# Kernel optimization log

Measured on AMD Instinct MI355X. Metric: run time of the kernel, lower is better.

Reference implementation:

```python
import jax, jax.numpy as jnp
import numpy as np

B, U, D, SKIP = 2048, 1024, 1024, 24

def setup_inputs() -> dict:
    key = jax.random.key(0)
    ks = jax.random.split(key, 8)
    return {
        "inputs": jax.random.normal(ks[0], (B, D), dtype=jnp.float32),
        "h_tm1": jax.random.normal(ks[1], (B, 4 * U), dtype=jnp.float32),
        "c_tm1": jax.random.normal(ks[2], (B, U), dtype=jnp.float32),
        "step": jnp.zeros((B, 1), dtype=jnp.float32),
        "prev_h": jax.random.normal(ks[3], (B, U * SKIP), dtype=jnp.float32),
        "kernel": jax.random.normal(ks[4], (D, 4 * U), dtype=jnp.float32) * (1.0 / np.sqrt(D)),
        "recurrent_kernel": jax.random.normal(ks[5], (U, 4 * U), dtype=jnp.float32) * (1.0 / np.sqrt(U)),
        "kernel2": jax.random.normal(ks[6], (U, U), dtype=jnp.float32) * (1.0 / np.sqrt(U)),
        "bias": jnp.zeros((4 * U,), dtype=jnp.float32),
        "bias2": jnp.zeros((U,), dtype=jnp.float32),
        "s0": jnp.float32(0.5),
    }

def reference(inputs, h_tm1, c_tm1, step, prev_h, kernel, recurrent_kernel, kernel2, bias, bias2, s0):
    units = kernel2.shape[0]
    # split previous 'h' state into its four gate-history blocks [B, U] each
    h_parts = jnp.stack(jnp.split(h_tm1, 4, axis=1), axis=0)          # [4, B, U]
    rk = recurrent_kernel.reshape(units, 4, units)                     # [U, 4, U]
    # fused per-gate recurrent matmuls: r[g] = h_parts[g] @ recurrent_kernel[:, g*U:(g+1)*U]
    r = jnp.einsum('gbu,ugv->gbv', h_parts, rk)                        # [4, B, U]
    x = inputs @ kernel + bias                                         # [B, 4U]
    x_i, x_f, x_c, x_o = jnp.split(x, 4, axis=1)
    i = jax.nn.sigmoid(x_i + r[0])
    f = jax.nn.sigmoid(x_f + r[1])
    c = f * c_tm1 + i * jnp.tanh(x_c + r[2])
    o = jax.nn.sigmoid(x_o + r[3])
    h = o * jnp.tanh(c)
    new_h_skip = jax.nn.sigmoid(prev_h[:, :units] @ kernel2 + bias2)
    h = s0 * h + new_h_skip * (1 - s0)
    new_h_tm1 = jnp.concatenate([i, f, c, o], axis=1)
    new_prev_h = jnp.concatenate([prev_h[:, units:], h], axis=1)
    return (h, new_h_tm1, c, step + 1, new_prev_h)
```

## Files before the change

kernel.cpp:

```cpp
#include <hip/hip_runtime.h>
#include <hip/hip_bf16.h>
#include <stdint.h>

#define BB 2048
#define UU 1024
#define SKIPN 24

typedef __attribute__((ext_vector_type(8))) short short8;
typedef __attribute__((ext_vector_type(4))) float f32x4;
typedef __attribute__((ext_vector_type(4))) unsigned short ushort4_t;

static __device__ __forceinline__ float sigmoidf_(float x) {
    return 1.0f / (1.0f + __expf(-x));
}

static __device__ __forceinline__ void load_lds16(const void* g, void* l) {
    __builtin_amdgcn_global_load_lds((const __attribute__((address_space(1))) void*)g,
                                     (__attribute__((address_space(3))) void*)l, 16, 0, 0);
}

static __device__ __forceinline__ f32x4 ntl(const f32x4* p) {
    return __builtin_nontemporal_load(p);
}
static __device__ __forceinline__ void nts(f32x4* p, f32x4 v) {
    __builtin_nontemporal_store(v, p);
}

__global__ __launch_bounds__(256) void prep(
    const float* __restrict__ inputs, const float* __restrict__ h_tm1,
    const float* __restrict__ prev_h, const float* __restrict__ kernel,
    const float* __restrict__ rkernel, const float* __restrict__ kernel2,
    __hip_bfloat16* __restrict__ kt, __hip_bfloat16* __restrict__ rkt,
    __hip_bfloat16* __restrict__ k2t, __hip_bfloat16* __restrict__ xin,
    __hip_bfloat16* __restrict__ hb, __hip_bfloat16* __restrict__ ph0) {
    const int bid = blockIdx.x;
    if (bid < 9216) {
        __shared__ float tile[32][33];
        const float* src;
        __hip_bfloat16* dst;
        int C, local;
        if (bid < 4096)      { src = kernel;  dst = kt;  C = 4096; local = bid; }
        else if (bid < 8192) { src = rkernel; dst = rkt; C = 4096; local = bid - 4096; }
        else                 { src = kernel2; dst = k2t; C = 1024; local = bid - 8192; }
        const int xt = (C == 4096) ? 128 : 32;
        const int bc = (local % xt) * 32;
        const int br = (local / xt) * 32;
        const int tx = threadIdx.x & 31, ty = threadIdx.x >> 5;
#pragma unroll
        for (int i = 0; i < 32; i += 8)
            tile[ty + i][tx] = src[(size_t)(br + ty + i) * C + bc + tx];
        __syncthreads();
#pragma unroll
        for (int i = 0; i < 32; i += 8)
            dst[(size_t)(bc + ty + i) * 1024 + br + tx] = __float2bfloat16(tile[tx][ty + i]);
    } else {
        const int idx = (bid - 9216) * 256 + threadIdx.x;
        const float* src;
        __hip_bfloat16* dst;
        int off;
        if (idx < 524288) { dst = xin; off = idx; src = inputs + (size_t)off * 4; }
        else if (idx < 2621440) { off = idx - 524288; dst = hb; src = h_tm1 + (size_t)off * 4; }
        else {
            const int i = idx - 2621440;
            const int b = i >> 8, c4 = i & 255;
            off = i; dst = ph0;
            src = prev_h + (size_t)b * (UU * SKIPN) + c4 * 4;
        }
        const float4 v = *(const float4*)src;
        union { __hip_bfloat16 h[4]; ushort4_t u; } cv;
        cv.h[0] = __float2bfloat16(v.x);
        cv.h[1] = __float2bfloat16(v.y);
        cv.h[2] = __float2bfloat16(v.z);
        cv.h[3] = __float2bfloat16(v.w);
        *(ushort4_t*)(dst + (size_t)off * 4) = cv.u;
    }
}

__global__ __launch_bounds__(256) void mega5(
    const __hip_bfloat16* __restrict__ xin,
    const __hip_bfloat16* __restrict__ hb,
    const __hip_bfloat16* __restrict__ ph0,
    const __hip_bfloat16* __restrict__ kt,
    const __hip_bfloat16* __restrict__ rkt,
    const __hip_bfloat16* __restrict__ k2t,
    const float* __restrict__ prev_h, float* __restrict__ out_prev,
    __hip_bfloat16* __restrict__ pre) {
    const int bid = blockIdx.x;
    if (bid >= 640) {
        const int b = bid - 640;
        const f32x4* s = (const f32x4*)(prev_h + (size_t)b * 24576 + 1024);
        f32x4* d = (f32x4*)(out_prev + (size_t)b * 24576);
        int c = threadIdx.x;
#pragma unroll 1
        for (int it = 0; it < 5; ++it) {
            f32x4 v0 = ntl(s + c);
            f32x4 v1 = ntl(s + c + 256);
            f32x4 v2 = ntl(s + c + 512);
            f32x4 v3 = ntl(s + c + 768);
            nts(d + c, v0);
            nts(d + c + 256, v1);
            nts(d + c + 512, v2);
            nts(d + c + 768, v3);
            c += 1024;
        }
        {
            f32x4 v0 = ntl(s + c);
            f32x4 v1 = ntl(s + c + 256);
            f32x4 v2 = ntl(s + c + 512);
            nts(d + c, v0);
            nts(d + c + 256, v1);
            nts(d + c + 512, v2);
        }
        return;
    }
    const int gi = bid;
    const int g = gi % 5;
    const int t = gi / 5;
    const int v0 = (t & 7) * 128;
    const int b0 = (t >> 3) * 128;

    __shared__ char As[3 * 8192];
    __shared__ char Bs[3 * 8192];

    const int tid = threadIdx.x;
    const int lane = tid & 63;
    const int wid = tid >> 6;
    const int wrow = wid >> 1;
    const int wcol = wid & 1;

    const int srow = tid >> 2;
    const int sslot = tid & 3;
    const int kofs = ((sslot ^ (srow & 3)) << 3);
    const int ldst = wid * 1024;

    const int l15 = lane & 15;
    const int hi = lane >> 4;
    const int rswB = ((hi ^ (l15 & 3)) << 4);

    f32x4 acc[4][4];
#pragma unroll
    for (int m = 0; m < 4; m++)
#pragma unroll
        for (int n = 0; n < 4; n++) acc[m][n] = (f32x4){0.f, 0.f, 0.f, 0.f};

    const __hip_bfloat16* A1;
    const __hip_bfloat16* W1;
    const __hip_bfloat16* A2 = nullptr;
    const __hip_bfloat16* W2 = nullptr;
    int lda1;
    if (g < 4) {
        A1 = xin; lda1 = 1024;
        W1 = kt + (size_t)g * 1048576;
        A2 = hb + (size_t)g * 1024;
        W2 = rkt + (size_t)g * 1048576;
    } else {
        A1 = ph0; lda1 = 1024;
        W1 = k2t;
    }

#define BARRIER() asm volatile("s_barrier" ::: "memory")
#define WAITV(N) asm volatile("s_waitcnt vmcnt(" #N ")" ::: "memory")
#define WAITL0() asm volatile("s_waitcnt lgkmcnt(0)" ::: "memory")

#define KSEG(AB, LDA, WB)                                                          \
    {                                                                              \
        const __hip_bfloat16* Ar0 = (AB) + (size_t)(b0 + srow) * (LDA) + kofs;     \
        const __hip_bfloat16* Ar1 = (AB) + (size_t)(b0 + 64 + srow) * (LDA) + kofs;\
        const __hip_bfloat16* Wr0 = (WB) + (size_t)(v0 + srow) * 1024 + kofs;      \
        const __hip_bfloat16* Wr1 = (WB) + (size_t)(v0 + 64 + srow) * 1024 + kofs; \
        load_lds16(Ar0, As + ldst);                                                \
        load_lds16(Ar1, As + ldst + 4096);                                         \
        load_lds16(Wr0, Bs + ldst);                                                \
        load_lds16(Wr1, Bs + ldst + 4096);                                         \
        load_lds16(Ar0 + 32, As + 8192 + ldst);                                    \
        load_lds16(Ar1 + 32, As + 8192 + ldst + 4096);                             \
        load_lds16(Wr0 + 32, Bs + 8192 + ldst);                                    \
        load_lds16(Wr1 + 32, Bs + 8192 + ldst + 4096);                             \
        int cur = 0;                                                               \
        for (int t_ = 0; t_ < 32; ++t_) {                                          \
            char* Ac = As + cur * 8192;                                            \
            char* Bc = Bs + cur * 8192;                                            \
            if (t_ < 30) {                                                         \
                int nxt = cur + 2; if (nxt >= 3) nxt -= 3;                         \
                const int kn = (t_ + 2) * 32;                                      \
                char* An = As + nxt * 8192 + ldst;                                 \
                char* Bn = Bs + nxt * 8192 + ldst;                                 \
                load_lds16(Ar0 + kn, An);                                          \
                load_lds16(Ar1 + kn, An + 4096);                                   \
                load_lds16(Wr0 + kn, Bn);                                          \
                load_lds16(Wr1 + kn, Bn + 4096);                                   \
                WAITV(8);                                                          \
            } else if (t_ == 30) {                                                 \
                WAITV(4);                                                          \
            } else {                                                               \
                WAITV(0);                                                          \
            }                                                                      \
            BARRIER();                                                             \
            short8 af[4], bfr[4];                                                  \
            _Pragma("unroll")                                                      \
            for (int m = 0; m < 4; m++)                                            \
                af[m] = *(const short8*)(Ac + (wrow * 64 + m * 16 + l15) * 64 + rswB); \
            _Pragma("unroll")                                                      \
            for (int n = 0; n < 4; n++)                                            \
                bfr[n] = *(const short8*)(Bc + (wcol * 64 + n * 16 + l15) * 64 + rswB); \
            _Pragma("unroll")                                                      \
            for (int m = 0; m < 4; m++)                                            \
                _Pragma("unroll")                                                  \
                for (int n = 0; n < 4; n++)                                        \
                    acc[m][n] = __builtin_amdgcn_mfma_f32_16x16x32_bf16(af[m], bfr[n], acc[m][n], 0, 0, 0); \
            WAITL0();                                                              \
            BARRIER();                                                             \
            cur = (cur == 2) ? 0 : cur + 1;                                        \
        }                                                                          \
    }

    KSEG(A1, lda1, W1);
    if (g < 4) KSEG(A2, 4096, W2);
#undef KSEG

    __hip_bfloat16* P = pre + (size_t)g * 2097152;
#pragma unroll
    for (int m = 0; m < 4; m++) {
#pragma unroll
        for (int n = 0; n < 4; n++) {
            const int col = v0 + wcol * 64 + n * 16 + l15;
            const int row = b0 + wrow * 64 + m * 16 + hi * 4;
#pragma unroll
            for (int r = 0; r < 4; r++)
                P[(size_t)(row + r) * 1024 + col] = __float2bfloat16(acc[m][n][r]);
        }
    }
#undef BARRIER
#undef WAITV
#undef WAITL0
}

__global__ __launch_bounds__(256) void epilogue3(
    const __hip_bfloat16* __restrict__ pre,
    const float* __restrict__ c_tm1, const float* __restrict__ bias,
    const float* __restrict__ bias2, const float* __restrict__ s0p,
    const float* __restrict__ step, float* __restrict__ out_h,
    float* __restrict__ out_ht, float* __restrict__ out_c,
    float* __restrict__ out_step, float* __restrict__ out_prev, int write_tail) {
    const int idx = blockIdx.x * 256 + threadIdx.x;
    const int b = idx >> 7;
    const int v = (idx & 127) * 8;
    const size_t bv = (size_t)b * 1024 + v;

    union u8 { short8 s; unsigned short u[8]; };
    u8 pi, pf, pc, po, ps;
    pi.s = *(const short8*)(pre + bv);
    pf.s = *(const short8*)(pre + 2097152 + bv);
    pc.s = *(const short8*)(pre + 4194304 + bv);
    po.s = *(const short8*)(pre + 6291456 + bv);
    ps.s = *(const short8*)(pre + 8388608 + bv);
    const float s0 = s0p[0];

    float hv[8], iv8[8], fv8[8], cn8[8], ov8[8];
#pragma unroll
    for (int j = 0; j < 4; j++) {
    }
#pragma unroll
    for (int j = 0; j < 8; j++) {
        const float pif = __bfloat162float(*(const __hip_bfloat16*)&pi.u[j]) + bias[v + j];
        const float pff = __bfloat162float(*(const __hip_bfloat16*)&pf.u[j]) + bias[1024 + v + j];
        const float pcf = __bfloat162float(*(const __hip_bfloat16*)&pc.u[j]) + bias[2048 + v + j];
        const float pof = __bfloat162float(*(const __hip_bfloat16*)&po.u[j]) + bias[3072 + v + j];
        const float psf = __bfloat162float(*(const __hip_bfloat16*)&ps.u[j]) + bias2[v + j];
        const float ct = c_tm1[bv + j];
        const float iv = sigmoidf_(pif);
        const float fv = sigmoidf_(pff);
        const float cn = fv * ct + iv * tanhf(pcf);
        const float ov = sigmoidf_(pof);
        const float sk = sigmoidf_(psf);
        hv[j] = s0 * (ov * tanhf(cn)) + sk * (1.0f - s0);
        iv8[j] = iv; fv8[j] = fv; cn8[j] = cn; ov8[j] = ov;
    }
#pragma unroll
    for (int q = 0; q < 2; q++) {
        const int o = q * 4;
        *(float4*)(out_h + bv + o) = make_float4(hv[o], hv[o+1], hv[o+2], hv[o+3]);
        *(float4*)(out_c + bv + o) = make_float4(cn8[o], cn8[o+1], cn8[o+2], cn8[o+3]);
        float* ht = out_ht + (size_t)b * 4096 + v + o;
        *(float4*)(ht) = make_float4(iv8[o], iv8[o+1], iv8[o+2], iv8[o+3]);
        *(float4*)(ht + 1024) = make_float4(fv8[o], fv8[o+1], fv8[o+2], fv8[o+3]);
        *(float4*)(ht + 2048) = make_float4(cn8[o], cn8[o+1], cn8[o+2], cn8[o+3]);
        *(float4*)(ht + 3072) = make_float4(ov8[o], ov8[o+1], ov8[o+2], ov8[o+3]);
        if (write_tail)
            *(float4*)(out_prev + (size_t)b * 24576 + 23552 + v + o) =
                make_float4(hv[o], hv[o+1], hv[o+2], hv[o+3]);
    }
    if (idx < 2048) out_step[idx] = step[idx] + 1.0f;
}

__global__ __launch_bounds__(256) void shift_only(
    const float* __restrict__ prev_h, const float* __restrict__ out_h,
    float* __restrict__ out_prev) {
    const int b = blockIdx.x;
    float4* d = (float4*)(out_prev + (size_t)b * 24576);
    const float4* s1 = (const float4*)(prev_h + (size_t)b * 24576 + 1024);
    const float4* s2 = (const float4*)(out_h + (size_t)b * 1024);
    for (int c = threadIdx.x; c < 6144; c += 256)
        d[c] = (c < 5888) ? s1[c] : s2[c - 5888];
}

extern "C" void kernel_launch(void* const* d_in, const int* in_sizes, int n_in,
                              void* d_out, int out_size, void* d_ws, size_t ws_size,
                              hipStream_t stream) {
    (void)in_sizes; (void)n_in; (void)out_size;
    const float* inputs = (const float*)d_in[0];
    const float* h_tm1 = (const float*)d_in[1];
    const float* c_tm1 = (const float*)d_in[2];
    const float* step = (const float*)d_in[3];
    const float* prev_h = (const float*)d_in[4];
    const float* kernel = (const float*)d_in[5];
    const float* rkernel = (const float*)d_in[6];
    const float* kernel2 = (const float*)d_in[7];
    const float* bias = (const float*)d_in[8];
    const float* bias2 = (const float*)d_in[9];
    const float* s0 = (const float*)d_in[10];

    float* out = (float*)d_out;
    float* out_h = out;
    float* out_ht = out + 2097152;
    float* out_c = out + 10485760;
    float* out_step = out + 12582912;
    float* out_prev = out + 12584960;

    const size_t NEED = 44040192 + 20971520;
    const int fits = (ws_size >= NEED);
    char* scr = fits ? (char*)d_ws : (char*)out_prev;
    __hip_bfloat16* kt = (__hip_bfloat16*)(scr + 0);
    __hip_bfloat16* rkt = (__hip_bfloat16*)(scr + 8388608);
    __hip_bfloat16* k2t = (__hip_bfloat16*)(scr + 16777216);
    __hip_bfloat16* xin = (__hip_bfloat16*)(scr + 18874368);
    __hip_bfloat16* hb = (__hip_bfloat16*)(scr + 23068672);
    __hip_bfloat16* ph0 = (__hip_bfloat16*)(scr + 39845888);
    __hip_bfloat16* pre = (__hip_bfloat16*)(scr + 44040192);

    prep<<<21504, 256, 0, stream>>>(inputs, h_tm1, prev_h, kernel, rkernel, kernel2,
                                    kt, rkt, k2t, xin, hb, ph0);
    if (fits) {
        mega5<<<2688, 256, 0, stream>>>(xin, hb, ph0, kt, rkt, k2t, prev_h, out_prev, pre);
        epilogue3<<<1024, 256, 0, stream>>>(pre, c_tm1, bias, bias2, s0, step,
                                            out_h, out_ht, out_c, out_step, out_prev, 1);
    } else {
        mega5<<<640, 256, 0, stream>>>(xin, hb, ph0, kt, rkt, k2t, prev_h, out_prev, pre);
        epilogue3<<<1024, 256, 0, stream>>>(pre, c_tm1, bias, bias2, s0, step,
                                            out_h, out_ht, out_c, out_step, out_prev, 0);
        shift_only<<<2048, 256, 0, stream>>>(prev_h, out_h, out_prev);
    }
}
```

Before: 161.7 us.

## Interleave prev_h shift copy into GEMM K-loop instead of separate copy blocks

The large prev_h shift copy used to run in 2048 dedicated blocks appended to the GEMM grid. Now most of that copy is spread across the 640 GEMM blocks, each issuing one nontemporal load and store per K-iteration alongside its LDS prefetches. A further 128 copy-only blocks handle the remainder with bounds checks. The aim is to hide copy bandwidth behind matmul compute. In exchange the vmcnt waits are loosened, extra registers are used, and the copy now competes with the GEMM's own memory traffic.

```diff
diff --git a/kernel.cpp b/kernel.cpp
--- a/kernel.cpp
+++ b/kernel.cpp
@@ -5,6 +5,7 @@
 #define BB 2048
 #define UU 1024
 #define SKIPN 24
+#define TOTC 12582656
 
 typedef __attribute__((ext_vector_type(8))) short short8;
 typedef __attribute__((ext_vector_type(4))) float f32x4;
@@ -76,7 +77,12 @@
     }
 }
 
-__global__ __launch_bounds__(256) void mega5(
+#define BARRIER() asm volatile("s_barrier" ::: "memory")
+#define WAITV(N) asm volatile("s_waitcnt vmcnt(" #N ")" ::: "memory")
+#define WAITL0() asm volatile("s_waitcnt lgkmcnt(0)" ::: "memory")
+
+template <int DC>
+__global__ __launch_bounds__(256) void mega10(
     const __hip_bfloat16* __restrict__ xin,
     const __hip_bfloat16* __restrict__ hb,
     const __hip_bfloat16* __restrict__ ph0,
@@ -86,30 +92,26 @@
     const float* __restrict__ prev_h, float* __restrict__ out_prev,
     __hip_bfloat16* __restrict__ pre) {
     const int bid = blockIdx.x;
-    if (bid >= 640) {
-        const int b = bid - 640;
-        const f32x4* s = (const f32x4*)(prev_h + (size_t)b * 24576 + 1024);
-        f32x4* d = (f32x4*)(out_prev + (size_t)b * 24576);
-        int c = threadIdx.x;
+    const int tid = threadIdx.x;
+    const f32x4* sb4 = (const f32x4*)(prev_h + 1024);
+    f32x4* db4 = (f32x4*)out_prev;
+
+    if (DC && bid >= 640) {
+        const int base = 9437184 + (bid - 640) * 24576;
 #pragma unroll 1
-        for (int it = 0; it < 5; ++it) {
-            f32x4 v0 = ntl(s + c);
-            f32x4 v1 = ntl(s + c + 256);
-            f32x4 v2 = ntl(s + c + 512);
-            f32x4 v3 = ntl(s + c + 768);
-            nts(d + c, v0);
-            nts(d + c + 256, v1);
-            nts(d + c + 512, v2);
-            nts(d + c + 768, v3);
-            c += 1024;
-        }
-        {
-            f32x4 v0 = ntl(s + c);
-            f32x4 v1 = ntl(s + c + 256);
-            f32x4 v2 = ntl(s + c + 512);
-            nts(d + c, v0);
-            nts(d + c + 256, v1);
-            nts(d + c + 512, v2);
+        for (int it = 0; it < 24; ++it) {
+            const int i0 = base + it * 1024 + tid;
+            const int i1 = i0 + 256, i2 = i0 + 512, i3 = i0 + 768;
+            const bool k0 = i0 < TOTC, k1 = i1 < TOTC, k2 = i2 < TOTC, k3 = i3 < TOTC;
+            f32x4 v0 = {}, v1 = {}, v2 = {}, v3 = {};
+            if (k0) v0 = ntl(sb4 + i0);
+            if (k1) v1 = ntl(sb4 + i1);
+            if (k2) v2 = ntl(sb4 + i2);
+            if (k3) v3 = ntl(sb4 + i3);
+            if (k0) nts(db4 + i0, v0);
+            if (k1) nts(db4 + i1, v1);
+            if (k2) nts(db4 + i2, v2);
+            if (k3) nts(db4 + i3, v3);
         }
         return;
     }
@@ -119,10 +121,15 @@
     const int v0 = (t & 7) * 128;
     const int b0 = (t >> 3) * 128;
 
+    int cpb1 = 0, cpb2 = 0;
+    if (DC) {
+        if (g < 4) { const int kk = t * 4 + g; cpb1 = kk * 16384; cpb2 = cpb1 + 8192; }
+        else       { cpb1 = 8388608 + t * 8192; }
+    }
+
     __shared__ char As[3 * 8192];
     __shared__ char Bs[3 * 8192];
 
-    const int tid = threadIdx.x;
     const int lane = tid & 63;
     const int wid = tid >> 6;
     const int wrow = wid >> 1;
@@ -158,11 +165,7 @@
         W1 = k2t;
     }
 
-#define BARRIER() asm volatile("s_barrier" ::: "memory")
-#define WAITV(N) asm volatile("s_waitcnt vmcnt(" #N ")" ::: "memory")
-#define WAITL0() asm volatile("s_waitcnt lgkmcnt(0)" ::: "memory")
-
-#define KSEG(AB, LDA, WB)                                                          \
+#define KSEG(AB, LDA, WB, CPB, CPON)                                               \
     {                                                                              \
         const __hip_bfloat16* Ar0 = (AB) + (size_t)(b0 + srow) * (LDA) + kofs;     \
         const __hip_bfloat16* Ar1 = (AB) + (size_t)(b0 + 64 + srow) * (LDA) + kofs;\
@@ -176,10 +179,21 @@
         load_lds16(Ar1 + 32, As + 8192 + ldst + 4096);                             \
         load_lds16(Wr0 + 32, Bs + 8192 + ldst);                                    \
         load_lds16(Wr1 + 32, Bs + 8192 + ldst + 4096);                             \
+        f32x4 creg0 = {}, creg1 = {};                                              \
         int cur = 0;                                                               \
+        _Pragma("unroll 2")                                                        \
         for (int t_ = 0; t_ < 32; ++t_) {                                          \
             char* Ac = As + cur * 8192;                                            \
             char* Bc = Bs + cur * 8192;                                            \
+            if (DC && (CPON)) {                                                    \
+                if (t_ & 1) {                                                      \
+                    nts(db4 + (CPB) + (t_ - 1) * 256 + tid, creg0);                \
+                    creg1 = ntl(sb4 + (CPB) + t_ * 256 + tid);                     \
+                } else {                                                           \
+                    if (t_ > 0) nts(db4 + (CPB) + (t_ - 1) * 256 + tid, creg1);    \
+                    creg0 = ntl(sb4 + (CPB) + t_ * 256 + tid);                     \
+                }                                                                  \
+            }                                                                      \
             if (t_ < 30) {                                                         \
                 int nxt = cur + 2; if (nxt >= 3) nxt -= 3;                         \
                 const int kn = (t_ + 2) * 32;                                      \
@@ -189,11 +203,11 @@
                 load_lds16(Ar1 + kn, An + 4096);                                   \
                 load_lds16(Wr0 + kn, Bn);                                          \
                 load_lds16(Wr1 + kn, Bn + 4096);                                   \
-                WAITV(8);                                                          \
+                if (DC && (CPON)) { WAITV(9); } else { WAITV(8); }                 \
             } else if (t_ == 30) {                                                 \
-                WAITV(4);                                                          \
+                if (DC && (CPON)) { WAITV(9); } else { WAITV(4); }                 \
             } else {                                                               \
-                WAITV(0);                                                          \
+                if (DC && (CPON)) { WAITV(9); } else { WAITV(0); }                 \
             }                                                                      \
             BARRIER();                                                             \
             short8 af[4], bfr[4];                                                  \
@@ -212,10 +226,11 @@
             BARRIER();                                                             \
             cur = (cur == 2) ? 0 : cur + 1;                                        \
         }                                                                          \
-    }
-
-    KSEG(A1, lda1, W1);
-    if (g < 4) KSEG(A2, 4096, W2);
+        if (DC && (CPON)) nts(db4 + (CPB) + 31 * 256 + tid, creg1);                \
+    }
+
+    KSEG(A1, lda1, W1, cpb1, 1);
+    if (g < 4) KSEG(A2, 4096, W2, cpb2, 1);
 #undef KSEG
 
     __hip_bfloat16* P = pre + (size_t)g * 2097152;
@@ -230,9 +245,6 @@
                 P[(size_t)(row + r) * 1024 + col] = __float2bfloat16(acc[m][n][r]);
         }
     }
-#undef BARRIER
-#undef WAITV
-#undef WAITL0
 }
 
 __global__ __launch_bounds__(256) void epilogue3(
@@ -257,9 +269,6 @@
     const float s0 = s0p[0];
 
     float hv[8], iv8[8], fv8[8], cn8[8], ov8[8];
-#pragma unroll
-    for (int j = 0; j < 4; j++) {
-    }
 #pragma unroll
     for (int j = 0; j < 8; j++) {
         const float pif = __bfloat162float(*(const __hip_bfloat16*)&pi.u[j]) + bias[v + j];
@@ -341,11 +350,13 @@
     prep<<<21504, 256, 0, stream>>>(inputs, h_tm1, prev_h, kernel, rkernel, kernel2,
                                     kt, rkt, k2t, xin, hb, ph0);
     if (fits) {
-        mega5<<<2688, 256, 0, stream>>>(xin, hb, ph0, kt, rkt, k2t, prev_h, out_prev, pre);
+        mega10<1><<<768, 256, 0, stream>>>(xin, hb, ph0, kt, rkt, k2t,
+                                           prev_h, out_prev, pre);
         epilogue3<<<1024, 256, 0, stream>>>(pre, c_tm1, bias, bias2, s0, step,
                                             out_h, out_ht, out_c, out_step, out_prev, 1);
     } else {
-        mega5<<<640, 256, 0, stream>>>(xin, hb, ph0, kt, rkt, k2t, prev_h, out_prev, pre);
+        mega10<0><<<640, 256, 0, stream>>>(xin, hb, ph0, kt, rkt, k2t,
+                                           prev_h, out_prev, pre);
         epilogue3<<<1024, 256, 0, stream>>>(pre, c_tm1, bias, bias2, s0, step,
                                             out_h, out_ht, out_c, out_step, out_prev, 0);
         shift_only<<<2048, 256, 0, stream>>>(prev_h, out_h, out_prev);
```

New measurement: 203.3 us. +25.7%, slower.

## Replace direct global-to-LDS loads with register-staged double-buffered GEMM pipeline

Applied to the files above, without the earlier changes.

The GEMM main loop stops using global_load_lds async copies into a triple-buffered LDS ring. Tiles are now prefetched two steps ahead into registers and written into a two-stage LDS double buffer after each step's MFMAs. One barrier per step remains. LDS use drops from 48KB to 32KB per block, which may allow more resident blocks, but it adds register pressure and extra VGPR-to-LDS store instructions.

```diff
diff --git a/kernel.cpp b/kernel.cpp
--- a/kernel.cpp
+++ b/kernel.cpp
@@ -12,11 +12,6 @@
 
 static __device__ __forceinline__ float sigmoidf_(float x) {
     return 1.0f / (1.0f + __expf(-x));
-}
-
-static __device__ __forceinline__ void load_lds16(const void* g, void* l) {
-    __builtin_amdgcn_global_load_lds((const __attribute__((address_space(1))) void*)g,
-                                     (__attribute__((address_space(3))) void*)l, 16, 0, 0);
 }
 
 static __device__ __forceinline__ f32x4 ntl(const f32x4* p) {
@@ -76,7 +71,11 @@
     }
 }
 
-__global__ __launch_bounds__(256) void mega5(
+#define BARRIER() asm volatile("s_barrier" ::: "memory")
+#define WAITL0() asm volatile("s_waitcnt lgkmcnt(0)" ::: "memory")
+
+template <int DC>
+__global__ __launch_bounds__(256) void mega12(
     const __hip_bfloat16* __restrict__ xin,
     const __hip_bfloat16* __restrict__ hb,
     const __hip_bfloat16* __restrict__ ph0,
@@ -86,11 +85,12 @@
     const float* __restrict__ prev_h, float* __restrict__ out_prev,
     __hip_bfloat16* __restrict__ pre) {
     const int bid = blockIdx.x;
-    if (bid >= 640) {
+    const int tid = threadIdx.x;
+    if (DC && bid >= 640) {
         const int b = bid - 640;
         const f32x4* s = (const f32x4*)(prev_h + (size_t)b * 24576 + 1024);
         f32x4* d = (f32x4*)(out_prev + (size_t)b * 24576);
-        int c = threadIdx.x;
+        int c = tid;
 #pragma unroll 1
         for (int it = 0; it < 5; ++it) {
             f32x4 v0 = ntl(s + c);
@@ -119,10 +119,9 @@
     const int v0 = (t & 7) * 128;
     const int b0 = (t >> 3) * 128;
 
-    __shared__ char As[3 * 8192];
-    __shared__ char Bs[3 * 8192];
-
-    const int tid = threadIdx.x;
+    __shared__ char As[2 * 8192];
+    __shared__ char Bs[2 * 8192];
+
     const int lane = tid & 63;
     const int wid = tid >> 6;
     const int wrow = wid >> 1;
@@ -131,7 +130,7 @@
     const int srow = tid >> 2;
     const int sslot = tid & 3;
     const int kofs = ((sslot ^ (srow & 3)) << 3);
-    const int ldst = wid * 1024;
+    const int wofs = tid * 16;
 
     const int l15 = lane & 15;
     const int hi = lane >> 4;
@@ -158,44 +157,35 @@
         W1 = k2t;
     }
 
-#define BARRIER() asm volatile("s_barrier" ::: "memory")
-#define WAITV(N) asm volatile("s_waitcnt vmcnt(" #N ")" ::: "memory")
-#define WAITL0() asm volatile("s_waitcnt lgkmcnt(0)" ::: "memory")
-
 #define KSEG(AB, LDA, WB)                                                          \
     {                                                                              \
         const __hip_bfloat16* Ar0 = (AB) + (size_t)(b0 + srow) * (LDA) + kofs;     \
         const __hip_bfloat16* Ar1 = (AB) + (size_t)(b0 + 64 + srow) * (LDA) + kofs;\
         const __hip_bfloat16* Wr0 = (WB) + (size_t)(v0 + srow) * 1024 + kofs;      \
         const __hip_bfloat16* Wr1 = (WB) + (size_t)(v0 + 64 + srow) * 1024 + kofs; \
-        load_lds16(Ar0, As + ldst);                                                \
-        load_lds16(Ar1, As + ldst + 4096);                                         \
-        load_lds16(Wr0, Bs + ldst);                                                \
-        load_lds16(Wr1, Bs + ldst + 4096);                                         \
-        load_lds16(Ar0 + 32, As + 8192 + ldst);                                    \
-        load_lds16(Ar1 + 32, As + 8192 + ldst + 4096);                             \
-        load_lds16(Wr0 + 32, Bs + 8192 + ldst);                                    \
-        load_lds16(Wr1 + 32, Bs + 8192 + ldst + 4096);                             \
-        int cur = 0;                                                               \
+        f32x4 sA0_0, sA1_0, sB0_0, sB1_0, sA0_1, sA1_1, sB0_1, sB1_1;              \
+        sA0_0 = *(const f32x4*)(Ar0);       sA1_0 = *(const f32x4*)(Ar1);          \
+        sB0_0 = *(const f32x4*)(Wr0);       sB1_0 = *(const f32x4*)(Wr1);          \
+        sA0_1 = *(const f32x4*)(Ar0 + 32);  sA1_1 = *(const f32x4*)(Ar1 + 32);     \
+        sB0_1 = *(const f32x4*)(Wr0 + 32);  sB1_1 = *(const f32x4*)(Wr1 + 32);     \
+        *(f32x4*)(As + wofs) = sA0_0;        *(f32x4*)(As + 4096 + wofs) = sA1_0;  \
+        *(f32x4*)(Bs + wofs) = sB0_0;        *(f32x4*)(Bs + 4096 + wofs) = sB1_0;  \
+        WAITL0(); BARRIER();                                                       \
+        _Pragma("unroll 2")                                                        \
         for (int t_ = 0; t_ < 32; ++t_) {                                          \
+            const int cur = t_ & 1;                                                \
             char* Ac = As + cur * 8192;                                            \
             char* Bc = Bs + cur * 8192;                                            \
-            if (t_ < 30) {                                                         \
-                int nxt = cur + 2; if (nxt >= 3) nxt -= 3;                         \
+            if (t_ + 2 < 32) {          \
                 const int kn = (t_ + 2) * 32;                                      \
-                char* An = As + nxt * 8192 + ldst;                                 \
-                char* Bn = Bs + nxt * 8192 + ldst;                                 \
-                load_lds16(Ar0 + kn, An);                                          \
-                load_lds16(Ar1 + kn, An + 4096);                                   \
-                load_lds16(Wr0 + kn, Bn);                                          \
-                load_lds16(Wr1 + kn, Bn + 4096);                                   \
-                WAITV(8);                                                          \
-            } else if (t_ == 30) {                                                 \
-                WAITV(4);                                                          \
-            } else {                                                               \
-                WAITV(0);                                                          \
+                if (cur == 0) {                                                    \
+                    sA0_0 = *(const f32x4*)(Ar0 + kn); sA1_0 = *(const f32x4*)(Ar1 + kn); \
+                    sB0_0 = *(const f32x4*)(Wr0 + kn); sB1_0 = *(const f32x4*)(Wr1 + kn); \
+                } else {                                                           \
+                    sA0_1 = *(const f32x4*)(Ar0 + kn); sA1_1 = *(const f32x4*)(Ar1 + kn); \
+                    sB0_1 = *(const f32x4*)(Wr0 + kn); sB1_1 = *(const f32x4*)(Wr1 + kn); \
+                }                                                                  \
             }                                                                      \
-            BARRIER();                                                             \
             short8 af[4], bfr[4];                                                  \
             _Pragma("unroll")                                                      \
             for (int m = 0; m < 4; m++)                                            \
@@ -208,9 +198,19 @@
                 _Pragma("unroll")                                                  \
                 for (int n = 0; n < 4; n++)                                        \
                     acc[m][n] = __builtin_amdgcn_mfma_f32_16x16x32_bf16(af[m], bfr[n], acc[m][n], 0, 0, 0); \
+            if (t_ + 1 < 32) {    \
+                char* Aw = As + (cur ^ 1) * 8192;                                  \
+                char* Bw = Bs + (cur ^ 1) * 8192;                                  \
+                if (cur == 0) {                                                    \
+                    *(f32x4*)(Aw + wofs) = sA0_1; *(f32x4*)(Aw + 4096 + wofs) = sA1_1; \
+                    *(f32x4*)(Bw + wofs) = sB0_1; *(f32x4*)(Bw + 4096 + wofs) = sB1_1; \
+                } else {                                                           \
+                    *(f32x4*)(Aw + wofs) = sA0_0; *(f32x4*)(Aw + 4096 + wofs) = sA1_0; \
+                    *(f32x4*)(Bw + wofs) = sB0_0; *(f32x4*)(Bw + 4096 + wofs) = sB1_0; \
+                }                                                                  \
+            }                                                                      \
             WAITL0();                                                              \
             BARRIER();                                                             \
-            cur = (cur == 2) ? 0 : cur + 1;                                        \
         }                                                                          \
     }
 
@@ -230,9 +230,6 @@
                 P[(size_t)(row + r) * 1024 + col] = __float2bfloat16(acc[m][n][r]);
         }
     }
-#undef BARRIER
-#undef WAITV
-#undef WAITL0
 }
 
 __global__ __launch_bounds__(256) void epilogue3(
@@ -257,9 +254,6 @@
     const float s0 = s0p[0];
 
     float hv[8], iv8[8], fv8[8], cn8[8], ov8[8];
-#pragma unroll
-    for (int j = 0; j < 4; j++) {
-    }
 #pragma unroll
     for (int j = 0; j < 8; j++) {
         const float pif = __bfloat162float(*(const __hip_bfloat16*)&pi.u[j]) + bias[v + j];
@@ -341,11 +335,13 @@
     prep<<<21504, 256, 0, stream>>>(inputs, h_tm1, prev_h, kernel, rkernel, kernel2,
                                     kt, rkt, k2t, xin, hb, ph0);
     if (fits) {
-        mega5<<<2688, 256, 0, stream>>>(xin, hb, ph0, kt, rkt, k2t, prev_h, out_prev, pre);
+        mega12<1><<<2688, 256, 0, stream>>>(xin, hb, ph0, kt, rkt, k2t,
+                                            prev_h, out_prev, pre);
         epilogue3<<<1024, 256, 0, stream>>>(pre, c_tm1, bias, bias2, s0, step,
                                             out_h, out_ht, out_c, out_step, out_prev, 1);
     } else {
-        mega5<<<640, 256, 0, stream>>>(xin, hb, ph0, kt, rkt, k2t, prev_h, out_prev, pre);
+        mega12<0><<<640, 256, 0, stream>>>(xin, hb, ph0, kt, rkt, k2t,
+                                           prev_h, out_prev, pre);
         epilogue3<<<1024, 256, 0, stream>>>(pre, c_tm1, bias, bias2, s0, step,
                                             out_h, out_ht, out_c, out_step, out_prev, 0);
         shift_only<<<2048, 256, 0, stream>>>(prev_h, out_h, out_prev);
```

Result: slower. 166.9 us (+3.2%).
